# Kernel optimization log

Measured on AMD Instinct MI355X. Metric: run time of the kernel, lower is better.

## Reference

```python
import jax, jax.numpy as jnp
import numpy as np

NEG_SLOPE = 0.2  # PyG GATConv default


def gat_layer(x, W, att_src, att_dst, bias, src, dst, concat):
    # x: [N, F_in]; W: [F_in, H*C]; att_src/att_dst: [H, C]; bias: [H*C] or [C]
    N = x.shape[0]
    H, C = att_src.shape
    h = (x @ W).reshape(N, H, C)                       # [N, H, C]
    a_s = jnp.einsum('nhc,hc->nh', h, att_src)         # [N, H]
    a_d = jnp.einsum('nhc,hc->nh', h, att_dst)
    e = jax.nn.leaky_relu(a_s[src] + a_d[dst], NEG_SLOPE)  # [E, H]
    # segment softmax over incoming edges of each destination node
    m = jax.ops.segment_max(e, dst, num_segments=N)
    m = jnp.where(jnp.isfinite(m), m, 0.0)
    ee = jnp.exp(e - m[dst])
    s = jax.ops.segment_sum(ee, dst, num_segments=N)
    alpha = ee / (s[dst] + 1e-16)                      # [E, H]
    out = jax.ops.segment_sum(h[src] * alpha[:, :, None], dst, num_segments=N)  # [N, H, C]
    out = out.reshape(N, H * C) if concat else out.mean(axis=1)
    return out + bias


def setup_inputs() -> dict:
    key = jax.random.key(0)
    ks = jax.random.split(key, 16)
    N, E, F_IN, NC = 100000, 3200000, 256, 40
    H, C = 8, 8  # hidden GATConv: heads=8, out=8 -> width 64
    inp = {}
    inp['features'] = jax.random.normal(ks[0], (N, F_IN), dtype=jnp.float32)
    inp['edge_index'] = jax.random.randint(ks[1], (2, E), 0, N, dtype=jnp.int64)
    def p(k, shape):
        return jax.random.normal(k, shape, dtype=jnp.float32) * 0.1
    # layer 0: in 256 -> 8 heads x 8 (concat -> 64)
    inp['W0'] = p(ks[2], (F_IN, H * C)); inp['as0'] = p(ks[3], (H, C)); inp['ad0'] = p(ks[4], (H, C)); inp['b0'] = jnp.zeros((H * C,), jnp.float32)
    # layer 1: 64 -> 8 heads x 8 (concat -> 64)
    inp['W1'] = p(ks[5], (H * C, H * C)); inp['as1'] = p(ks[6], (H, C)); inp['ad1'] = p(ks[7], (H, C)); inp['b1'] = jnp.zeros((H * C,), jnp.float32)
    # layer 2: 64 -> 1 head x n_classes (mean/no-concat)
    inp['W2'] = p(ks[8], (H * C, NC)); inp['as2'] = p(ks[9], (1, NC)); inp['ad2'] = p(ks[10], (1, NC)); inp['b2'] = jnp.zeros((NC,), jnp.float32)
    return inp


def reference(features, edge_index, W0, as0, ad0, b0, W1, as1, ad1, b1, W2, as2, ad2, b2):
    N = features.shape[0]
    loops = jnp.arange(N, dtype=edge_index.dtype)  # PyG GATConv adds self-loops by default
    src = jnp.concatenate([edge_index[0], loops])
    dst = jnp.concatenate([edge_index[1], loops])
    x = gat_layer(features, W0, as0, ad0, b0, src, dst, True)
    x = gat_layer(x, W1, as1, ad1, b1, src, dst, True)
    x = gat_layer(x, W2, as2, ad2, b2, src, dst, False)
    return jax.nn.log_softmax(x, axis=-1)
```

## Files before the change

### kernel.cpp

```cpp
#include <hip/hip_runtime.h>
#include <hip/hip_bf16.h>

#define NEG_SLOPE 0.2f
#define LOG2E 1.44269504f
#define EPB 8192
#define MAXBUCK 800

typedef __attribute__((ext_vector_type(8))) short short8;
typedef __attribute__((ext_vector_type(4))) float f32x4;

__device__ __forceinline__ unsigned short f2bf(float x) {
    unsigned u = __float_as_uint(x);
    unsigned r = (u + 0x7FFFu + ((u >> 16) & 1u)) >> 16;
    return (unsigned short)r;
}

__device__ __forceinline__ float fexp2(float x) {
    return __builtin_amdgcn_exp2f(x);
}


__global__ __launch_bounds__(512) void bucket_hist_k(
    const int* __restrict__ dsts, int* __restrict__ bcnt,
    int* __restrict__ bhist, int E, int nbuck) {
    __shared__ int lh[MAXBUCK];
    int t = threadIdx.x;
    for (int i = t; i < nbuck; i += 512) lh[i] = 0;
    __syncthreads();
    int base = blockIdx.x * EPB;
    int cnt = E - base;
    if (cnt > EPB) cnt = EPB;
    int nq = cnt >> 2;
    const int4* d4p = (const int4*)(dsts + base);
    for (int i = t; i < nq; i += 512) {
        int4 d = d4p[i];
        atomicAdd(&lh[d.x >> 7], 1);
        atomicAdd(&lh[d.y >> 7], 1);
        atomicAdd(&lh[d.z >> 7], 1);
        atomicAdd(&lh[d.w >> 7], 1);
    }
    for (int i = (nq << 2) + t; i < cnt; i += 512)
        atomicAdd(&lh[dsts[base + i] >> 7], 1);
    __syncthreads();
    int* bh = bhist + (size_t)blockIdx.x * MAXBUCK;
    for (int i = t; i < nbuck; i += 512) {
        int c = lh[i];
        bh[i] = c;
        if (c) atomicAdd(&bcnt[i], c);
    }
}

__global__ __launch_bounds__(512) void bucket_scan_k(
    const int* __restrict__ bcnt, int* __restrict__ bptrE,
    int* __restrict__ bcurE, int nbuck) {
    __shared__ int csum[512];
    int t = threadIdx.x;
    int i0 = t * 4;
    int v0 = 0, v1 = 0, v2 = 0, v3 = 0;
    if (i0 < nbuck) v0 = bcnt[i0];
    if (i0 + 1 < nbuck) v1 = bcnt[i0 + 1];
    if (i0 + 2 < nbuck) v2 = bcnt[i0 + 2];
    if (i0 + 3 < nbuck) v3 = bcnt[i0 + 3];
    int s = v0 + v1 + v2 + v3;
    csum[t] = s;
    __syncthreads();
    for (int off = 1; off < 512; off <<= 1) {
        int x = (t >= off) ? csum[t - off] : 0;
        __syncthreads();
        csum[t] += x;
        __syncthreads();
    }
    int base = csum[t] - s;
    if (i0 < nbuck)     { bptrE[i0] = base;     bcurE[i0] = base; }     base += v0;
    if (i0 + 1 < nbuck) { bptrE[i0 + 1] = base; bcurE[i0 + 1] = base; } base += v1;
    if (i0 + 2 < nbuck) { bptrE[i0 + 2] = base; bcurE[i0 + 2] = base; } base += v2;
    if (i0 + 3 < nbuck) { bptrE[i0 + 3] = base; bcurE[i0 + 3] = base; }
}

__global__ __launch_bounds__(512) void bscatter_k(
    const int* __restrict__ srcs, const int* __restrict__ dsts,
    const int* __restrict__ bhist, int* __restrict__ bcurE,
    int* __restrict__ pairs, int E, int nbuck) {
    __shared__ int lh[MAXBUCK];
    __shared__ int lbase[MAXBUCK];
    int t = threadIdx.x;
    const int* bh = bhist + (size_t)blockIdx.x * MAXBUCK;
    for (int i = t; i < nbuck; i += 512) {
        int c = bh[i];
        lbase[i] = c ? atomicAdd(&bcurE[i], c) : 0;
        lh[i] = 0;
    }
    __syncthreads();
    int base = blockIdx.x * EPB;
    int cnt = E - base;
    if (cnt > EPB) cnt = EPB;
    int nq = cnt >> 2;
    const int4* d4p = (const int4*)(dsts + base);
    const int4* s4p = (const int4*)(srcs + base);
    for (int i = t; i < nq; i += 512) {
        int4 d = d4p[i];
        int4 s = s4p[i];
        int b0 = d.x >> 7, b1 = d.y >> 7, b2 = d.z >> 7, b3 = d.w >> 7;
        int r0 = atomicAdd(&lh[b0], 1);
        int r1 = atomicAdd(&lh[b1], 1);
        int r2 = atomicAdd(&lh[b2], 1);
        int r3 = atomicAdd(&lh[b3], 1);
        pairs[lbase[b0] + r0] = (s.x << 7) | (d.x & 127);
        pairs[lbase[b1] + r1] = (s.y << 7) | (d.y & 127);
        pairs[lbase[b2] + r2] = (s.z << 7) | (d.z & 127);
        pairs[lbase[b3] + r3] = (s.w << 7) | (d.w & 127);
    }
    for (int i = (nq << 2) + t; i < cnt; i += 512) {
        int s = srcs[base + i], d = dsts[base + i];
        int r = atomicAdd(&lh[d >> 7], 1);
        pairs[lbase[d >> 7] + r] = (s << 7) | (d & 127);
    }
}

__global__ __launch_bounds__(256) void bucket_sort_k(
    const int* __restrict__ pairs, const int* __restrict__ bptrE,
    const int* __restrict__ bcurE, int* __restrict__ row_ptr,
    int* __restrict__ csr_src, int N, int Etot) {
    __shared__ int lh[128];
    __shared__ int sc[128];
    int b = blockIdx.x;
    int n0 = b << 7;
    int t = threadIdx.x;
    if (t < 128) lh[t] = 0;
    __syncthreads();
    int e0 = bptrE[b], e1 = bcurE[b];
    for (int e = e0 + t; e < e1; e += 256)
        atomicAdd(&lh[pairs[e] & 127], 1);
    __syncthreads();
    if (t < 128) sc[t] = lh[t];
    __syncthreads();
    for (int off = 1; off < 128; off <<= 1) {
        int x = (t < 128 && t >= off) ? sc[t - off] : 0;
        __syncthreads();
        if (t < 128) sc[t] += x;
        __syncthreads();
    }
    if (t < 128) {
        int cntv = lh[t];
        int excl = sc[t] - cntv;
        int n = n0 + t;
        int rp = e0 + n0 + t + excl;
        if (n < N) {
            row_ptr[n] = rp;
            csr_src[rp] = n << 7;
        }
        lh[t] = rp + 1;
    }
    __syncthreads();
    for (int e = e0 + t; e < e1; e += 256) {
        int p = pairs[e];
        int pos = atomicAdd(&lh[p & 127], 1);
        csr_src[pos] = p & ~127;
    }
    if (b == 0 && t == 0) row_ptr[N] = Etot;
}


template <int K>
__global__ __launch_bounds__(256) void gemm_pack8_k(
    const float* __restrict__ x, const float* __restrict__ W,
    const float* __restrict__ a_src, const float* __restrict__ a_dst,
    char* __restrict__ hrec, float* __restrict__ asb,
    float* __restrict__ adb, int N) {
    constexpr int NT = 4;
    constexpr int KT = K / 32;
    constexpr size_t WF_BYTES = (size_t)KT * NT * 64 * 8 * sizeof(short);
    constexpr size_t H_BYTES = (size_t)64 * 65 * sizeof(float);
    __shared__ alignas(16) char smem[WF_BYTES > H_BYTES ? WF_BYTES : H_BYTES];
    short* Wf = (short*)smem;
    float* hL = (float*)smem;
    int tid = threadIdx.x;
    for (int f = tid; f < KT * NT * 64; f += 256) {
        int lane = f & 63;
        int ntk = f >> 6;
        int nt = ntk % NT, kt = ntk / NT;
        int q = lane >> 4, c = lane & 15;
        int n = nt * 16 + c;
        int k0 = kt * 32 + q * 8;
        short8 frag;
        #pragma unroll
        for (int j = 0; j < 8; ++j)
            frag[j] = (short)f2bf(W[(size_t)(k0 + j) * 64 + n]);
        *(short8*)&Wf[f * 8] = frag;
    }
    __syncthreads();
    int wave = tid >> 6, lane = tid & 63;
    int q = lane >> 4, c = lane & 15;
    int m0 = blockIdx.x * 64 + wave * 16;
    int arow = m0 + c;
    int arl = arow < N ? arow : N - 1;
    f32x4 acc[NT] = {};
    for (int kt = 0; kt < KT; ++kt) {
        const float* xp = x + (size_t)arl * K + kt * 32 + q * 8;
        float4 a0 = *(const float4*)xp;
        float4 a1 = *(const float4*)(xp + 4);
        float av[8] = {a0.x, a0.y, a0.z, a0.w, a1.x, a1.y, a1.z, a1.w};
        short8 af;
        #pragma unroll
        for (int j = 0; j < 8; ++j) af[j] = (short)f2bf(av[j]);
        #pragma unroll
        for (int nt = 0; nt < NT; ++nt) {
            short8 bf = *(const short8*)&Wf[((kt * NT + nt) * 64 + lane) * 8];
            acc[nt] = __builtin_amdgcn_mfma_f32_16x16x32_bf16(af, bf, acc[nt],
                                                              0, 0, 0);
        }
    }
    __syncthreads();
    int lrow = wave * 16 + q * 4;
    #pragma unroll
    for (int nt = 0; nt < NT; ++nt)
        #pragma unroll
        for (int reg = 0; reg < 4; ++reg)
            hL[(lrow + reg) * 65 + nt * 16 + c] = acc[nt][reg];
    __syncthreads();
    #pragma unroll
    for (int it = 0; it < 2; ++it) {
        int id = it * 256 + tid;
        int ln = id >> 3, hd = id & 7;
        int gn = blockIdx.x * 64 + ln;
        if (gn >= N) continue;
        const float* hp = &hL[ln * 65 + hd * 8];
        float as = 0.f, ad = 0.f;
        float hv[8];
        #pragma unroll
        for (int j = 0; j < 8; ++j) {
            hv[j] = hp[j];
            as += hv[j] * a_src[hd * 8 + j];
            ad += hv[j] * a_dst[hd * 8 + j];
        }
        adb[gn * 8 + hd] = ad * LOG2E;
        asb[gn * 8 + hd] = as * LOG2E;
        unsigned short u[8];
        #pragma unroll
        for (int j = 0; j < 8; ++j) u[j] = f2bf(hv[j]);
        uint4 pk;
        pk.x = (unsigned)u[0] | ((unsigned)u[1] << 16);
        pk.y = (unsigned)u[2] | ((unsigned)u[3] << 16);
        pk.z = (unsigned)u[4] | ((unsigned)u[5] << 16);
        pk.w = (unsigned)u[6] | ((unsigned)u[7] << 16);
        *(uint4*)(hrec + (size_t)gn * 128 + hd * 16) = pk;
    }
}


__global__ __launch_bounds__(256) void gemm_pack40_k(
    const float* __restrict__ x, const float* __restrict__ W,
    const float* __restrict__ a_src, const float* __restrict__ a_dst,
    char* __restrict__ rec40, float* __restrict__ adb, int N) {
    constexpr int K = 64, NT = 3, KT = 2;
    constexpr size_t WF_BYTES = (size_t)KT * NT * 64 * 8 * sizeof(short);
    constexpr size_t H_BYTES = (size_t)64 * 41 * sizeof(float);
    __shared__ alignas(16) char smem[WF_BYTES > H_BYTES ? WF_BYTES : H_BYTES];
    short* Wf = (short*)smem;
    float* hL = (float*)smem;
    int tid = threadIdx.x;
    for (int f = tid; f < KT * NT * 64; f += 256) {
        int lane = f & 63;
        int ntk = f >> 6;
        int nt = ntk % NT, kt = ntk / NT;
        int q = lane >> 4, c = lane & 15;
        int n = nt * 16 + c;
        int k0 = kt * 32 + q * 8;
        short8 frag;
        #pragma unroll
        for (int j = 0; j < 8; ++j) {
            float v = (n < 40) ? W[(size_t)(k0 + j) * 40 + n] : 0.f;
            frag[j] = (short)f2bf(v);
        }
        *(short8*)&Wf[f * 8] = frag;
    }
    __syncthreads();
    int wave = tid >> 6, lane = tid & 63;
    int q = lane >> 4, c = lane & 15;
    int m0 = blockIdx.x * 64 + wave * 16;
    int arow = m0 + c;
    int arl = arow < N ? arow : N - 1;
    f32x4 acc[NT] = {};
    for (int kt = 0; kt < KT; ++kt) {
        const float* xp = x + (size_t)arl * K + kt * 32 + q * 8;
        float4 a0 = *(const float4*)xp;
        float4 a1 = *(const float4*)(xp + 4);
        float av[8] = {a0.x, a0.y, a0.z, a0.w, a1.x, a1.y, a1.z, a1.w};
        short8 af;
        #pragma unroll
        for (int j = 0; j < 8; ++j) af[j] = (short)f2bf(av[j]);
        #pragma unroll
        for (int nt = 0; nt < NT; ++nt) {
            short8 bf = *(const short8*)&Wf[((kt * NT + nt) * 64 + lane) * 8];
            acc[nt] = __builtin_amdgcn_mfma_f32_16x16x32_bf16(af, bf, acc[nt],
                                                              0, 0, 0);
        }
    }
    __syncthreads();
    int lrow = wave * 16 + q * 4;
    #pragma unroll
    for (int nt = 0; nt < NT; ++nt) {
        int n = nt * 16 + c;
        if (n >= 40) continue;
        #pragma unroll
        for (int reg = 0; reg < 4; ++reg)
            hL[(lrow + reg) * 41 + n] = acc[nt][reg];
    }
    __syncthreads();
    int ln = tid >> 2, sub = tid & 3;
    int gn = blockIdx.x * 64 + ln;
    float pas = 0.f, pad = 0.f;
    if (gn < N) {
        for (int j = sub; j < 40; j += 4) {
            float hv = hL[ln * 41 + j];
            pas += hv * a_src[j];
            pad += hv * a_dst[j];
        }
    }
    pas += __shfl_xor(pas, 1); pas += __shfl_xor(pas, 2);
    pad += __shfl_xor(pad, 1); pad += __shfl_xor(pad, 2);
    if (gn < N && sub == 0) {
        *(float*)(rec40 + (size_t)gn * 128 + 80) = pas * LOG2E;
        adb[gn] = pad * LOG2E;
    }
    for (int i = tid; i < 64 * 40; i += 256) {
        int n2 = i / 40, ch = i % 40;
        int g2 = blockIdx.x * 64 + n2;
        if (g2 < N)
            *(unsigned short*)(rec40 + (size_t)g2 * 128 + ch * 2) =
                f2bf(hL[n2 * 41 + ch]);
    }
}


#define G64(SUF, JB)                                                          \
    int sv##SUF = __builtin_amdgcn_ds_bpermute((JB) * 4 + g4, sv);            \
    float w##SUF = wb[(JB) + wofs];                                           \
    uint4 hv##SUF =                                                           \
        *(const uint4*)(gbase + (size_t)(unsigned)sv##SUF + hoff);

#define FMA8(SUF, LS)                                                         \
    LS;                                                                       \
    acc0 = fmaf(w##SUF, __uint_as_float(hv##SUF.x << 16), acc0);              \
    acc1 = fmaf(w##SUF, __uint_as_float(hv##SUF.x & 0xFFFF0000u), acc1);      \
    acc2 = fmaf(w##SUF, __uint_as_float(hv##SUF.y << 16), acc2);              \
    acc3 = fmaf(w##SUF, __uint_as_float(hv##SUF.y & 0xFFFF0000u), acc3);      \
    acc4 = fmaf(w##SUF, __uint_as_float(hv##SUF.z << 16), acc4);              \
    acc5 = fmaf(w##SUF, __uint_as_float(hv##SUF.z & 0xFFFF0000u), acc5);      \
    acc6 = fmaf(w##SUF, __uint_as_float(hv##SUF.w << 16), acc6);              \
    acc7 = fmaf(w##SUF, __uint_as_float(hv##SUF.w & 0xFFFF0000u), acc7);

__global__ __launch_bounds__(256) void aggr64_k(
    const char* __restrict__ hrec, const float* __restrict__ asb,
    const float* __restrict__ adb, const int* __restrict__ row_ptr,
    const int* __restrict__ csr_src, const float* __restrict__ bias,
    float* __restrict__ out, int N) {
    __shared__ float wlds[4 * 544];
    int wave = threadIdx.x >> 6;
    int node = blockIdx.x * 4 + wave;
    if (node >= N) return;
    int lane = threadIdx.x & 63;
    const char* gbase = hrec;
    float* wb = wlds + wave * 544;
    int g4 = (lane >> 3) * 4;
    int hoff = (lane & 7) * 16;
    int wofs = (lane & 7) * 68 + (lane >> 3);
    int beg = row_ptr[node], end = row_ptr[node + 1];
    float4 adv0 = *(const float4*)(adb + (size_t)node * 8);
    float4 adv1 = *(const float4*)(adb + (size_t)node * 8 + 4);
    float acc0 = 0.f, acc1 = 0.f, acc2 = 0.f, acc3 = 0.f;
    float acc4 = 0.f, acc5 = 0.f, acc6 = 0.f, acc7 = 0.f;
    float lpart = 0.f;
    for (int i0 = beg; i0 < end; i0 += 64) {
        int tail = end - i0;
        int sv = csr_src[i0 + (lane < tail ? lane : 0)];
        int cnt = tail < 64 ? tail : 64;
        {
            const float* asp =
                (const float*)((const char*)asb + (((unsigned)sv) >> 2));
            float4 s0 = *(const float4*)asp;
            float4 s1 = *(const float4*)(asp + 4);
            float w0 = s0.x + adv0.x; w0 = fmaxf(w0, NEG_SLOPE * w0); w0 = fexp2(w0);
            float w1 = s0.y + adv0.y; w1 = fmaxf(w1, NEG_SLOPE * w1); w1 = fexp2(w1);
            float w2 = s0.z + adv0.z; w2 = fmaxf(w2, NEG_SLOPE * w2); w2 = fexp2(w2);
            float w3 = s0.w + adv0.w; w3 = fmaxf(w3, NEG_SLOPE * w3); w3 = fexp2(w3);
            float w4 = s1.x + adv1.x; w4 = fmaxf(w4, NEG_SLOPE * w4); w4 = fexp2(w4);
            float w5 = s1.y + adv1.y; w5 = fmaxf(w5, NEG_SLOPE * w5); w5 = fexp2(w5);
            float w6 = s1.z + adv1.z; w6 = fmaxf(w6, NEG_SLOPE * w6); w6 = fexp2(w6);
            float w7 = s1.w + adv1.w; w7 = fmaxf(w7, NEG_SLOPE * w7); w7 = fexp2(w7);
            if (lane >= cnt) {
                w0 = 0.f; w1 = 0.f; w2 = 0.f; w3 = 0.f;
                w4 = 0.f; w5 = 0.f; w6 = 0.f; w7 = 0.f;
            }
            wb[lane]          = w0;
            wb[68 + lane]     = w1;
            wb[2 * 68 + lane] = w2;
            wb[3 * 68 + lane] = w3;
            wb[4 * 68 + lane] = w4;
            wb[5 * 68 + lane] = w5;
            wb[6 * 68 + lane] = w6;
            wb[7 * 68 + lane] = w7;
        }
        int j = 0;
        for (; j + 32 <= cnt; j += 32) {
            G64(A, j) G64(B, j + 8) G64(C, j + 16) G64(D, j + 24)
            FMA8(A, lpart += wA) FMA8(B, lpart += wB)
            FMA8(C, lpart += wC) FMA8(D, lpart += wD)
        }
        for (; j < cnt; j += 8) {
            G64(A, j)
            FMA8(A, lpart += wA)
        }
    }
    #pragma unroll
    for (int m = 8; m <= 32; m <<= 1) {
        acc0 += __shfl_xor(acc0, m);
        acc1 += __shfl_xor(acc1, m);
        acc2 += __shfl_xor(acc2, m);
        acc3 += __shfl_xor(acc3, m);
        acc4 += __shfl_xor(acc4, m);
        acc5 += __shfl_xor(acc5, m);
        acc6 += __shfl_xor(acc6, m);
        acc7 += __shfl_xor(acc7, m);
        lpart += __shfl_xor(lpart, m);
    }
    if (lane < 8) {
        float denom = lpart + 1e-16f;
        const float4 b0 = *(const float4*)(bias + lane * 8);
        const float4 b1 = *(const float4*)(bias + lane * 8 + 4);
        float4 o0, o1;
        o0.x = acc0 / denom + b0.x;
        o0.y = acc1 / denom + b0.y;
        o0.z = acc2 / denom + b0.z;
        o0.w = acc3 / denom + b0.w;
        o1.x = acc4 / denom + b1.x;
        o1.y = acc5 / denom + b1.y;
        o1.z = acc6 / denom + b1.z;
        o1.w = acc7 / denom + b1.w;
        float* op = out + (size_t)node * 64 + lane * 8;
        *(float4*)op = o0;
        *(float4*)(op + 4) = o1;
    }
}


#define G40(SUF, JB)                                                          \
    int sv##SUF = __builtin_amdgcn_ds_bpermute((JB) * 4 + g4, sv);            \
    float w##SUF = wb[(JB) + gof];                                            \
    uint4 hv##SUF =                                                           \
        *(const uint4*)(gbase + (size_t)(unsigned)sv##SUF + hoff);

__global__ __launch_bounds__(256) void aggr40_k(
    const char* __restrict__ rec40, const float* __restrict__ adb,
    const int* __restrict__ row_ptr, const int* __restrict__ csr_src,
    const float* __restrict__ bias, float* __restrict__ out, int N) {
    __shared__ float wlds[4 * 104];
    int wave = threadIdx.x >> 6;
    int node = blockIdx.x * 4 + wave;
    if (node >= N) return;
    int lane = threadIdx.x & 63;
    const char* gbase = rec40;
    float* wb = wlds + wave * 104;
    float* epi = wb + 64;
    int g4 = (lane >> 3) * 4;
    int sub = lane & 7;
    int hoff = (sub < 5 ? sub : 0) * 16;
    int gof = lane >> 3;
    int beg = row_ptr[node], end = row_ptr[node + 1];
    float ad = adb[node];
    float acc0 = 0.f, acc1 = 0.f, acc2 = 0.f, acc3 = 0.f;
    float acc4 = 0.f, acc5 = 0.f, acc6 = 0.f, acc7 = 0.f;
    float lpart = 0.f;
    for (int i0 = beg; i0 < end; i0 += 64) {
        int tail = end - i0;
        int sv = csr_src[i0 + (lane < tail ? lane : 0)];
        int cnt = tail < 64 ? tail : 64;
        float as = *(const float*)(rec40 + (size_t)(unsigned)sv + 80);
        float v = as + ad;
        v = fmaxf(v, NEG_SLOPE * v);
        float wv = fexp2(v);
        wv = (lane < cnt) ? wv : 0.f;
        lpart += wv;
        wb[lane] = wv;
        int j = 0;
        for (; j + 32 <= cnt; j += 32) {
            G40(A, j) G40(B, j + 8) G40(C, j + 16) G40(D, j + 24)
            FMA8(A, ) FMA8(B, ) FMA8(C, ) FMA8(D, )
        }
        for (; j < cnt; j += 8) {
            G40(A, j)
            FMA8(A, )
        }
    }
    #pragma unroll
    for (int m = 8; m <= 32; m <<= 1) {
        acc0 += __shfl_xor(acc0, m);
        acc1 += __shfl_xor(acc1, m);
        acc2 += __shfl_xor(acc2, m);
        acc3 += __shfl_xor(acc3, m);
        acc4 += __shfl_xor(acc4, m);
        acc5 += __shfl_xor(acc5, m);
        acc6 += __shfl_xor(acc6, m);
        acc7 += __shfl_xor(acc7, m);
    }
    #pragma unroll
    for (int off = 32; off > 0; off >>= 1) lpart += __shfl_xor(lpart, off);
    float l = lpart;
    if (lane < 5) {
        *(float4*)&epi[lane * 8] = make_float4(acc0, acc1, acc2, acc3);
        *(float4*)&epi[lane * 8 + 4] = make_float4(acc4, acc5, acc6, acc7);
    }
    float accv = (lane < 40) ? epi[lane] : 0.f;
    float val = accv / (l + 1e-16f) + ((lane < 40) ? bias[lane] : 0.f);
    float mval = (lane < 40) ? val : -1e30f;
    #pragma unroll
    for (int off = 32; off > 0; off >>= 1)
        mval = fmaxf(mval, __shfl_xor(mval, off));
    float ex = (lane < 40) ? __expf(val - mval) : 0.f;
    #pragma unroll
    for (int off = 32; off > 0; off >>= 1) ex += __shfl_xor(ex, off);
    if (lane < 40)
        out[(size_t)node * 40 + lane] = val - mval - __logf(ex);
}


extern "C" void kernel_launch(void* const* d_in, const int* in_sizes, int n_in,
                              void* d_out, int out_size, void* d_ws,
                              size_t ws_size, hipStream_t stream) {
    const float* features = (const float*)d_in[0];
    const int* edge_index = (const int*)d_in[1];
    const float* W0 = (const float*)d_in[2];
    const float* as0 = (const float*)d_in[3];
    const float* ad0 = (const float*)d_in[4];
    const float* b0 = (const float*)d_in[5];
    const float* W1 = (const float*)d_in[6];
    const float* as1 = (const float*)d_in[7];
    const float* ad1 = (const float*)d_in[8];
    const float* b1 = (const float*)d_in[9];
    const float* W2 = (const float*)d_in[10];
    const float* as2 = (const float*)d_in[11];
    const float* ad2 = (const float*)d_in[12];
    const float* b2 = (const float*)d_in[13];

    int N = in_sizes[0] / 256;
    int E = in_sizes[1] / 2;
    int Etot = E + N;
    int nbuck = (N + 127) >> 7;
    const int* srcs = edge_index;
    const int* dsts = edge_index + E;

    float* ws = (float*)d_ws;
    float* Hbuf = ws;
    float* Abuf = Hbuf + (size_t)N * 64;
    float* adb  = Abuf + (size_t)N * 64;
    float* asb  = adb + (size_t)N * 8;
    char* hrec  = (char*)(asb + (size_t)N * 8);
    int* row_ptr = (int*)(hrec + (size_t)N * 128);
    int* bcnt    = row_ptr + (N + 2);
    int* bptrE   = bcnt + MAXBUCK;
    int* bcurE   = bptrE + MAXBUCK;
    int* csr_src = bcurE + MAXBUCK;
    int* bhist   = csr_src + Etot;
    int* pairs   = (int*)Hbuf;

    const int B = 256;
    int gAg = (N + 3) / 4;
    int gGm = (N + 63) / 64;
    int gSc = (E + EPB - 1) / EPB;

    (void)hipMemsetAsync(bcnt, 0, MAXBUCK * 4, stream);
    bucket_hist_k<<<gSc, 512, 0, stream>>>(dsts, bcnt, bhist, E, nbuck);
    bucket_scan_k<<<1, 512, 0, stream>>>(bcnt, bptrE, bcurE, nbuck);
    bscatter_k<<<gSc, 512, 0, stream>>>(srcs, dsts, bhist, bcurE, pairs, E,
                                        nbuck);
    bucket_sort_k<<<nbuck, B, 0, stream>>>(pairs, bptrE, bcurE, row_ptr,
                                           csr_src, N, Etot);

    gemm_pack8_k<256><<<gGm, B, 0, stream>>>(features, W0, as0, ad0, hrec,
                                             asb, adb, N);
    aggr64_k<<<gAg, B, 0, stream>>>(hrec, asb, adb, row_ptr, csr_src, b0,
                                    Abuf, N);

    gemm_pack8_k<64><<<gGm, B, 0, stream>>>(Abuf, W1, as1, ad1, hrec, asb,
                                            adb, N);
    aggr64_k<<<gAg, B, 0, stream>>>(hrec, asb, adb, row_ptr, csr_src, b1,
                                    Abuf, N);

    gemm_pack40_k<<<gGm, B, 0, stream>>>(Abuf, W2, as2, ad2, hrec, adb, N);
    aggr40_k<<<gAg, B, 0, stream>>>(hrec, adb, row_ptr, csr_src, b2,
                                    (float*)d_out, N);
}
```

Baseline: 552.1 us.

## Launch one-wave blocks per node in aggregation and widen bucket sort blocks

Aggregation kernels switch from 4-wave blocks (one wave per node) to single-wave 64-thread blocks with one node per block, so waves no longer wait on the slowest sibling and blocks can retire independently. The aggr64 edge-weight LDS layout changes from head-major padded rows to per-edge contiguous float4 pairs, which lets weights be written with vector stores and read at a stride of 8. The bucket sort kernel is widened to 512 threads, and edges-per-block in the histogram/scatter is halved for more parallelism. The cost is four times as many tiny blocks, which adds launch and scheduling overhead, and the stride-8 LDS reads may cause bank conflicts.

```diff
diff --git a/kernel.cpp b/kernel.cpp
--- a/kernel.cpp
+++ b/kernel.cpp
@@ -3,7 +3,7 @@
 
 #define NEG_SLOPE 0.2f
 #define LOG2E 1.44269504f
-#define EPB 8192
+#define EPB 4096
 #define MAXBUCK 800
 
 typedef __attribute__((ext_vector_type(8))) short short8;
@@ -117,7 +117,7 @@
     }
 }
 
-__global__ __launch_bounds__(256) void bucket_sort_k(
+__global__ __launch_bounds__(512) void bucket_sort_k(
     const int* __restrict__ pairs, const int* __restrict__ bptrE,
     const int* __restrict__ bcurE, int* __restrict__ row_ptr,
     int* __restrict__ csr_src, int N, int Etot) {
@@ -129,7 +129,7 @@
     if (t < 128) lh[t] = 0;
     __syncthreads();
     int e0 = bptrE[b], e1 = bcurE[b];
-    for (int e = e0 + t; e < e1; e += 256)
+    for (int e = e0 + t; e < e1; e += 512)
         atomicAdd(&lh[pairs[e] & 127], 1);
     __syncthreads();
     if (t < 128) sc[t] = lh[t];
@@ -152,7 +152,7 @@
         lh[t] = rp + 1;
     }
     __syncthreads();
-    for (int e = e0 + t; e < e1; e += 256) {
+    for (int e = e0 + t; e < e1; e += 512) {
         int p = pairs[e];
         int pos = atomicAdd(&lh[p & 127], 1);
         csr_src[pos] = p & ~127;
@@ -335,7 +335,7 @@
 
 #define G64(SUF, JB)                                                          \
     int sv##SUF = __builtin_amdgcn_ds_bpermute((JB) * 4 + g4, sv);            \
-    float w##SUF = wb[(JB) + wofs];                                           \
+    float w##SUF = wp[(JB) * 8];                                              \
     uint4 hv##SUF =                                                           \
         *(const uint4*)(gbase + (size_t)(unsigned)sv##SUF + hoff);
 
@@ -350,21 +350,19 @@
     acc6 = fmaf(w##SUF, __uint_as_float(hv##SUF.w << 16), acc6);              \
     acc7 = fmaf(w##SUF, __uint_as_float(hv##SUF.w & 0xFFFF0000u), acc7);
 
-__global__ __launch_bounds__(256) void aggr64_k(
+__global__ __launch_bounds__(64) void aggr64_k(
     const char* __restrict__ hrec, const float* __restrict__ asb,
     const float* __restrict__ adb, const int* __restrict__ row_ptr,
     const int* __restrict__ csr_src, const float* __restrict__ bias,
     float* __restrict__ out, int N) {
-    __shared__ float wlds[4 * 544];
-    int wave = threadIdx.x >> 6;
-    int node = blockIdx.x * 4 + wave;
+    __shared__ float wb[512];
+    int node = blockIdx.x;
     if (node >= N) return;
     int lane = threadIdx.x & 63;
     const char* gbase = hrec;
-    float* wb = wlds + wave * 544;
     int g4 = (lane >> 3) * 4;
     int hoff = (lane & 7) * 16;
-    int wofs = (lane & 7) * 68 + (lane >> 3);
+    const float* wp = wb + lane;
     int beg = row_ptr[node], end = row_ptr[node + 1];
     float4 adv0 = *(const float4*)(adb + (size_t)node * 8);
     float4 adv1 = *(const float4*)(adb + (size_t)node * 8 + 4);
@@ -392,14 +390,8 @@
                 w0 = 0.f; w1 = 0.f; w2 = 0.f; w3 = 0.f;
                 w4 = 0.f; w5 = 0.f; w6 = 0.f; w7 = 0.f;
             }
-            wb[lane]          = w0;
-            wb[68 + lane]     = w1;
-            wb[2 * 68 + lane] = w2;
-            wb[3 * 68 + lane] = w3;
-            wb[4 * 68 + lane] = w4;
-            wb[5 * 68 + lane] = w5;
-            wb[6 * 68 + lane] = w6;
-            wb[7 * 68 + lane] = w7;
+            *(float4*)&wb[lane * 8] = make_float4(w0, w1, w2, w3);
+            *(float4*)&wb[lane * 8 + 4] = make_float4(w4, w5, w6, w7);
         }
         int j = 0;
         for (; j + 32 <= cnt; j += 32) {
@@ -450,18 +442,16 @@
     uint4 hv##SUF =                                                           \
         *(const uint4*)(gbase + (size_t)(unsigned)sv##SUF + hoff);
 
-__global__ __launch_bounds__(256) void aggr40_k(
+__global__ __launch_bounds__(64) void aggr40_k(
     const char* __restrict__ rec40, const float* __restrict__ adb,
     const int* __restrict__ row_ptr, const int* __restrict__ csr_src,
     const float* __restrict__ bias, float* __restrict__ out, int N) {
-    __shared__ float wlds[4 * 104];
-    int wave = threadIdx.x >> 6;
-    int node = blockIdx.x * 4 + wave;
+    __shared__ float wb[64];
+    __shared__ float epi[40];
+    int node = blockIdx.x;
     if (node >= N) return;
     int lane = threadIdx.x & 63;
     const char* gbase = rec40;
-    float* wb = wlds + wave * 104;
-    float* epi = wb + 64;
     int g4 = (lane >> 3) * 4;
     int sub = lane & 7;
     int hoff = (sub < 5 ? sub : 0) * 16;
@@ -564,7 +554,6 @@
     int* pairs   = (int*)Hbuf;
 
     const int B = 256;
-    int gAg = (N + 3) / 4;
     int gGm = (N + 63) / 64;
     int gSc = (E + EPB - 1) / EPB;
 
@@ -573,20 +562,20 @@
     bucket_scan_k<<<1, 512, 0, stream>>>(bcnt, bptrE, bcurE, nbuck);
     bscatter_k<<<gSc, 512, 0, stream>>>(srcs, dsts, bhist, bcurE, pairs, E,
                                         nbuck);
-    bucket_sort_k<<<nbuck, B, 0, stream>>>(pairs, bptrE, bcurE, row_ptr,
-                                           csr_src, N, Etot);
+    bucket_sort_k<<<nbuck, 512, 0, stream>>>(pairs, bptrE, bcurE, row_ptr,
+                                             csr_src, N, Etot);
 
     gemm_pack8_k<256><<<gGm, B, 0, stream>>>(features, W0, as0, ad0, hrec,
                                              asb, adb, N);
-    aggr64_k<<<gAg, B, 0, stream>>>(hrec, asb, adb, row_ptr, csr_src, b0,
-                                    Abuf, N);
+    aggr64_k<<<N, 64, 0, stream>>>(hrec, asb, adb, row_ptr, csr_src, b0,
+                                   Abuf, N);
 
     gemm_pack8_k<64><<<gGm, B, 0, stream>>>(Abuf, W1, as1, ad1, hrec, asb,
                                             adb, N);
-    aggr64_k<<<gAg, B, 0, stream>>>(hrec, asb, adb, row_ptr, csr_src, b1,
-                                    Abuf, N);
+    aggr64_k<<<N, 64, 0, stream>>>(hrec, asb, adb, row_ptr, csr_src, b1,
+                                   Abuf, N);
 
     gemm_pack40_k<<<gGm, B, 0, stream>>>(Abuf, W2, as2, ad2, hrec, adb, N);
-    aggr40_k<<<gAg, B, 0, stream>>>(hrec, adb, row_ptr, csr_src, b2,
-                                    (float*)d_out, N);
-}
+    aggr40_k<<<N, 64, 0, stream>>>(hrec, adb, row_ptr, csr_src, b2,
+                                   (float*)d_out, N);
+}
```

Result: slower. 571.8 us (+3.6%).

## Fuse bucket histogram into scatter using fixed-capacity buckets, scan afterward

Applied to the files above, without the earlier changes.

Replaces the separate histogram, scan and scatter passes with one scatter kernel that writes into fixed-capacity (CAP=8000) per-bucket regions via per-block atomic reservations. A small scan then computes the global bucket offsets for the final per-bucket sort. This removes one full pass over the destination array, the per-block histogram buffer and a memset. It also halves edges per block and doubles threads in the sort kernel. It risks overflow if any bucket of 128 nodes receives more than CAP edges, which is safe only because the degree distribution is uniform, and the pairs buffer must hold nbuck*CAP entries.

```diff
diff --git a/kernel.cpp b/kernel.cpp
--- a/kernel.cpp
+++ b/kernel.cpp
@@ -3,8 +3,9 @@
 
 #define NEG_SLOPE 0.2f
 #define LOG2E 1.44269504f
-#define EPB 8192
+#define EPB 4096
 #define MAXBUCK 800
+#define CAP 8000
 
 typedef __attribute__((ext_vector_type(8))) short short8;
 typedef __attribute__((ext_vector_type(4))) float f32x4;
@@ -20,10 +21,17 @@
 }
 
 
-__global__ __launch_bounds__(512) void bucket_hist_k(
-    const int* __restrict__ dsts, int* __restrict__ bcnt,
-    int* __restrict__ bhist, int E, int nbuck) {
+__global__ __launch_bounds__(256) void binit_k(int* __restrict__ bcurE,
+                                               int nbuck) {
+    int b = blockIdx.x * 256 + threadIdx.x;
+    if (b < nbuck) bcurE[b] = b * CAP;
+}
+
+__global__ __launch_bounds__(512) void bscatter_k(
+    const int* __restrict__ srcs, const int* __restrict__ dsts,
+    int* __restrict__ bcurE, int* __restrict__ pairs, int E, int nbuck) {
     __shared__ int lh[MAXBUCK];
+    __shared__ int lbase[MAXBUCK];
     int t = threadIdx.x;
     for (int i = t; i < nbuck; i += 512) lh[i] = 0;
     __syncthreads();
@@ -32,6 +40,7 @@
     if (cnt > EPB) cnt = EPB;
     int nq = cnt >> 2;
     const int4* d4p = (const int4*)(dsts + base);
+    const int4* s4p = (const int4*)(srcs + base);
     for (int i = t; i < nq; i += 512) {
         int4 d = d4p[i];
         atomicAdd(&lh[d.x >> 7], 1);
@@ -42,61 +51,12 @@
     for (int i = (nq << 2) + t; i < cnt; i += 512)
         atomicAdd(&lh[dsts[base + i] >> 7], 1);
     __syncthreads();
-    int* bh = bhist + (size_t)blockIdx.x * MAXBUCK;
     for (int i = t; i < nbuck; i += 512) {
         int c = lh[i];
-        bh[i] = c;
-        if (c) atomicAdd(&bcnt[i], c);
-    }
-}
-
-__global__ __launch_bounds__(512) void bucket_scan_k(
-    const int* __restrict__ bcnt, int* __restrict__ bptrE,
-    int* __restrict__ bcurE, int nbuck) {
-    __shared__ int csum[512];
-    int t = threadIdx.x;
-    int i0 = t * 4;
-    int v0 = 0, v1 = 0, v2 = 0, v3 = 0;
-    if (i0 < nbuck) v0 = bcnt[i0];
-    if (i0 + 1 < nbuck) v1 = bcnt[i0 + 1];
-    if (i0 + 2 < nbuck) v2 = bcnt[i0 + 2];
-    if (i0 + 3 < nbuck) v3 = bcnt[i0 + 3];
-    int s = v0 + v1 + v2 + v3;
-    csum[t] = s;
-    __syncthreads();
-    for (int off = 1; off < 512; off <<= 1) {
-        int x = (t >= off) ? csum[t - off] : 0;
-        __syncthreads();
-        csum[t] += x;
-        __syncthreads();
-    }
-    int base = csum[t] - s;
-    if (i0 < nbuck)     { bptrE[i0] = base;     bcurE[i0] = base; }     base += v0;
-    if (i0 + 1 < nbuck) { bptrE[i0 + 1] = base; bcurE[i0 + 1] = base; } base += v1;
-    if (i0 + 2 < nbuck) { bptrE[i0 + 2] = base; bcurE[i0 + 2] = base; } base += v2;
-    if (i0 + 3 < nbuck) { bptrE[i0 + 3] = base; bcurE[i0 + 3] = base; }
-}
-
-__global__ __launch_bounds__(512) void bscatter_k(
-    const int* __restrict__ srcs, const int* __restrict__ dsts,
-    const int* __restrict__ bhist, int* __restrict__ bcurE,
-    int* __restrict__ pairs, int E, int nbuck) {
-    __shared__ int lh[MAXBUCK];
-    __shared__ int lbase[MAXBUCK];
-    int t = threadIdx.x;
-    const int* bh = bhist + (size_t)blockIdx.x * MAXBUCK;
-    for (int i = t; i < nbuck; i += 512) {
-        int c = bh[i];
         lbase[i] = c ? atomicAdd(&bcurE[i], c) : 0;
         lh[i] = 0;
     }
     __syncthreads();
-    int base = blockIdx.x * EPB;
-    int cnt = E - base;
-    if (cnt > EPB) cnt = EPB;
-    int nq = cnt >> 2;
-    const int4* d4p = (const int4*)(dsts + base);
-    const int4* s4p = (const int4*)(srcs + base);
     for (int i = t; i < nq; i += 512) {
         int4 d = d4p[i];
         int4 s = s4p[i];
@@ -117,9 +77,38 @@
     }
 }
 
-__global__ __launch_bounds__(256) void bucket_sort_k(
-    const int* __restrict__ pairs, const int* __restrict__ bptrE,
-    const int* __restrict__ bcurE, int* __restrict__ row_ptr,
+__global__ __launch_bounds__(512) void bscan_k(
+    const int* __restrict__ bcurE, int* __restrict__ bstart, int nbuck) {
+    __shared__ int csum[512];
+    int t = threadIdx.x;
+    int i0 = t * 4;
+    int v0 = 0, v1 = 0, v2 = 0, v3 = 0;
+    if (i0 < nbuck) v0 = bcurE[i0] - i0 * CAP;
+    if (i0 + 1 < nbuck) v1 = bcurE[i0 + 1] - (i0 + 1) * CAP;
+    if (i0 + 2 < nbuck) v2 = bcurE[i0 + 2] - (i0 + 2) * CAP;
+    if (i0 + 3 < nbuck) v3 = bcurE[i0 + 3] - (i0 + 3) * CAP;
+    int s = v0 + v1 + v2 + v3;
+    csum[t] = s;
+    __syncthreads();
+    for (int off = 1; off < 512; off <<= 1) {
+        int x = (t >= off) ? csum[t - off] : 0;
+        __syncthreads();
+        csum[t] += x;
+        __syncthreads();
+    }
+    int base = csum[t] - s;
+    if (i0 < nbuck) bstart[i0] = base;
+    base += v0;
+    if (i0 + 1 < nbuck) bstart[i0 + 1] = base;
+    base += v1;
+    if (i0 + 2 < nbuck) bstart[i0 + 2] = base;
+    base += v2;
+    if (i0 + 3 < nbuck) bstart[i0 + 3] = base;
+}
+
+__global__ __launch_bounds__(512) void bucket_sort_k(
+    const int* __restrict__ pairs, const int* __restrict__ bcurE,
+    const int* __restrict__ bstart, int* __restrict__ row_ptr,
     int* __restrict__ csr_src, int N, int Etot) {
     __shared__ int lh[128];
     __shared__ int sc[128];
@@ -128,8 +117,8 @@
     int t = threadIdx.x;
     if (t < 128) lh[t] = 0;
     __syncthreads();
-    int e0 = bptrE[b], e1 = bcurE[b];
-    for (int e = e0 + t; e < e1; e += 256)
+    int e0c = b * CAP, e1c = bcurE[b];
+    for (int e = e0c + t; e < e1c; e += 512)
         atomicAdd(&lh[pairs[e] & 127], 1);
     __syncthreads();
     if (t < 128) sc[t] = lh[t];
@@ -140,11 +129,12 @@
         if (t < 128) sc[t] += x;
         __syncthreads();
     }
+    int e0g = bstart[b];
     if (t < 128) {
         int cntv = lh[t];
         int excl = sc[t] - cntv;
         int n = n0 + t;
-        int rp = e0 + n0 + t + excl;
+        int rp = e0g + n0 + t + excl;
         if (n < N) {
             row_ptr[n] = rp;
             csr_src[rp] = n << 7;
@@ -152,7 +142,7 @@
         lh[t] = rp + 1;
     }
     __syncthreads();
-    for (int e = e0 + t; e < e1; e += 256) {
+    for (int e = e0c + t; e < e1c; e += 512) {
         int p = pairs[e];
         int pos = atomicAdd(&lh[p & 127], 1);
         csr_src[pos] = p & ~127;
@@ -556,25 +546,22 @@
     float* asb  = adb + (size_t)N * 8;
     char* hrec  = (char*)(asb + (size_t)N * 8);
     int* row_ptr = (int*)(hrec + (size_t)N * 128);
-    int* bcnt    = row_ptr + (N + 2);
-    int* bptrE   = bcnt + MAXBUCK;
-    int* bcurE   = bptrE + MAXBUCK;
-    int* csr_src = bcurE + MAXBUCK;
-    int* bhist   = csr_src + Etot;
+    int* bcurE   = row_ptr + (N + 2);
+    int* bstart  = bcurE + MAXBUCK;
+    int* csr_src = bstart + MAXBUCK;
     int* pairs   = (int*)Hbuf;
 
     const int B = 256;
     int gAg = (N + 3) / 4;
     int gGm = (N + 63) / 64;
     int gSc = (E + EPB - 1) / EPB;
-
-    (void)hipMemsetAsync(bcnt, 0, MAXBUCK * 4, stream);
-    bucket_hist_k<<<gSc, 512, 0, stream>>>(dsts, bcnt, bhist, E, nbuck);
-    bucket_scan_k<<<1, 512, 0, stream>>>(bcnt, bptrE, bcurE, nbuck);
-    bscatter_k<<<gSc, 512, 0, stream>>>(srcs, dsts, bhist, bcurE, pairs, E,
-                                        nbuck);
-    bucket_sort_k<<<nbuck, B, 0, stream>>>(pairs, bptrE, bcurE, row_ptr,
-                                           csr_src, N, Etot);
+    int gBi = (nbuck + 255) / 256;
+
+    binit_k<<<gBi, B, 0, stream>>>(bcurE, nbuck);
+    bscatter_k<<<gSc, 512, 0, stream>>>(srcs, dsts, bcurE, pairs, E, nbuck);
+    bscan_k<<<1, 512, 0, stream>>>(bcurE, bstart, nbuck);
+    bucket_sort_k<<<nbuck, 512, 0, stream>>>(pairs, bcurE, bstart, row_ptr,
+                                             csr_src, N, Etot);
 
     gemm_pack8_k<256><<<gGm, B, 0, stream>>>(features, W0, as0, ad0, hrec,
                                              asb, adb, N);
```

New measurement: 554.3 us. Within noise of the previous version (+0.4%).
